# Kernel tuning notes

Hardware: AMD Instinct MI355X
Metric: run time of the kernel (lower is better)

## Reference

```python
import jax, jax.numpy as jnp
import numpy as np
from jax import lax

BATCH = 8192
HIDDEN = 128
N_POINTS = 8
MAX_STEPS = 8     # adaptive substep budget per output interval
RTOL, ATOL = 1e-3, 1e-4

# Dormand-Prince 5(4) tableau (FSAL)
A21 = 1/5
A31, A32 = 3/40, 9/40
A41, A42, A43 = 44/45, -56/15, 32/9
A51, A52, A53, A54 = 19372/6561, -25360/2187, 64448/6561, -212/729
A61, A62, A63, A64, A65 = 9017/3168, -355/33, 46732/5247, 49/176, -5103/18656
B1, B3, B4, B5, B6 = 35/384, 500/1113, 125/192, -2187/6784, 11/84
# error weights = b(5th) - b(4th)
E1 = 35/384 - 5179/57600
E3 = 500/1113 - 7571/16695
E4 = 125/192 - 393/640
E5 = -2187/6784 + 92097/339200
E6 = 11/84 - 187/2100
E7 = -1/40


def setup_inputs() -> dict:
    key = jax.random.key(0)
    ks = jax.random.split(key, 6)
    def xavier(k, fi, fo):
        return (jax.random.normal(k, (fi, fo)) * jnp.sqrt(2.0 / (fi + fo))).astype(jnp.float32)
    W1 = xavier(ks[0], 2, HIDDEN); b1 = jnp.zeros((HIDDEN,), jnp.float32)
    W2 = xavier(ks[1], HIDDEN, HIDDEN); b2 = jnp.zeros((HIDDEN,), jnp.float32)
    W3 = xavier(ks[2], HIDDEN, HIDDEN); b3 = jnp.zeros((HIDDEN,), jnp.float32)
    W4 = xavier(ks[3], HIDDEN, 2); b4 = jnp.zeros((2,), jnp.float32)
    x0 = jax.random.normal(ks[4], (BATCH, 2), jnp.float32)
    t = (jnp.arange(N_POINTS, dtype=jnp.float32) * 0.1)
    return {"x0": x0, "t": t, "W1": W1, "b1": b1, "W2": W2, "b2": b2,
            "W3": W3, "b3": b3, "W4": W4, "b4": b4}


def _odeint(x0, t, W1, b1, W2, b2, W3, b3, W4, b4):
    def f(y):  # autonomous dynamics: ODEFunc ignores t
        h = jax.nn.elu(y @ W1 + b1)
        h = jax.nn.elu(h @ W2 + b2)
        h = jax.nn.elu(h @ W3 + b3)
        return h @ W4 + b4

    def dopri5_step(y, h):
        k1 = f(y)
        k2 = f(y + h * (A21 * k1))
        k3 = f(y + h * (A31 * k1 + A32 * k2))
        k4 = f(y + h * (A41 * k1 + A42 * k2 + A43 * k3))
        k5 = f(y + h * (A51 * k1 + A52 * k2 + A53 * k3 + A54 * k4))
        k6 = f(y + h * (A61 * k1 + A62 * k2 + A63 * k3 + A64 * k4 + A65 * k5))
        y5 = y + h * (B1 * k1 + B3 * k3 + B4 * k4 + B5 * k5 + B6 * k6)
        k7 = f(y5)  # FSAL stage, used only for error estimate here
        err = h * (E1 * k1 + E3 * k3 + E4 * k4 + E5 * k5 + E6 * k6 + E7 * k7)
        tol = ATOL + RTOL * jnp.maximum(jnp.abs(y), jnp.abs(y5))
        err_norm = jnp.sqrt(jnp.mean((err / tol) ** 2))
        return y5, err_norm

    def solve_interval(carry, ts):
        y, h = carry
        t0, t1 = ts

        def body(c, _):
            y, tc, h = c
            remaining = t1 - tc
            done = remaining <= 1e-9
            h_eff = jnp.where(done, h, jnp.minimum(h, remaining))
            y5, err_norm = dopri5_step(y, h_eff)
            accept = (err_norm <= 1.0) & (~done)
            y = jnp.where(accept, y5, y)
            tc = jnp.where(accept, tc + h_eff, tc)
            factor = jnp.clip(0.9 * jnp.maximum(err_norm, 1e-10) ** (-0.2), 0.2, 10.0)
            h = jnp.where(done, h, h_eff * factor)
            return (y, tc, h), None

        (y, _, h), _ = lax.scan(body, (y, t0, h), None, length=MAX_STEPS)
        return (y, h), y

    h0 = (t[1] - t[0]) * 0.5
    (_, _), ys = lax.scan(solve_interval, (x0, h0), (t[:-1], t[1:]))
    return jnp.concatenate([x0[None], ys], axis=0)  # (n_points, batch, 2)


def reference(x0, t, W1, b1, W2, b2, W3, b3, W4, b4):
    return _odeint(x0, t, W1, b1, W2, b2, W3, b3, W4, b4)
```

## Files before the change

### kernel.cpp

```cpp
#include <hip/hip_runtime.h>
#include <stdint.h>

typedef unsigned int u32;
typedef unsigned long long u64;
typedef unsigned short u16;
typedef float f32x4 __attribute__((ext_vector_type(4)));
typedef float f32x2 __attribute__((ext_vector_type(2)));
typedef short short8 __attribute__((ext_vector_type(8)));
typedef unsigned int u32x2 __attribute__((ext_vector_type(2)));
typedef unsigned int u32x4 __attribute__((ext_vector_type(4)));

#define HID  128
#define MT   32
#define NWG  256
#define NTHR 512
#define LD   136

#define OFF_ESUM  0
#define OFF_CNT   512
#define OFF_WPACK 8192
#define OFF_W2TH  16384
#define OFF_W2TL  49152
#define OFF_W3TH  81920
#define OFF_W3TL  114688

constexpr float CA21 = (float)(1.0/5.0);
constexpr float CA31 = (float)(3.0/40.0),   CA32 = (float)(9.0/40.0);
constexpr float CA41 = (float)(44.0/45.0),  CA42 = (float)(-56.0/15.0), CA43 = (float)(32.0/9.0);
constexpr float CA51 = (float)(19372.0/6561.0), CA52 = (float)(-25360.0/2187.0);
constexpr float CA53 = (float)(64448.0/6561.0), CA54 = (float)(-212.0/729.0);
constexpr float CA61 = (float)(9017.0/3168.0),  CA62 = (float)(-355.0/33.0);
constexpr float CA63 = (float)(46732.0/5247.0), CA64 = (float)(49.0/176.0), CA65 = (float)(-5103.0/18656.0);
constexpr float CB1 = (float)(35.0/384.0), CB3 = (float)(500.0/1113.0), CB4 = (float)(125.0/192.0);
constexpr float CB5 = (float)(-2187.0/6784.0), CB6 = (float)(11.0/84.0);
constexpr float CE1 = (float)(35.0/384.0 - 5179.0/57600.0);
constexpr float CE3 = (float)(500.0/1113.0 - 7571.0/16695.0);
constexpr float CE4 = (float)(125.0/192.0 - 393.0/640.0);
constexpr float CE5 = (float)(-2187.0/6784.0 + 92097.0/339200.0);
constexpr float CE6 = (float)(11.0/84.0 - 187.0/2100.0);
constexpr float CE7 = (float)(-1.0/40.0);

template<int N> struct IC { static constexpr int v = N; };

__device__ __forceinline__ u16 f2bf(float x) {
  u32 u = __builtin_bit_cast(u32, x);
  u32 r = (u + 0x7FFFu + ((u >> 16) & 1u)) >> 16;
  return (u16)r;
}
__device__ __forceinline__ float bf2f(u16 b) {
  u32 u = ((u32)b) << 16;
  return __builtin_bit_cast(float, u);
}
__device__ __forceinline__ float eluf(float x) {
  return x > 0.f ? x : (__expf(x) - 1.f);
}
__device__ __forceinline__ u32 cvtpk(float a, float b) {
  u32 r; asm("v_cvt_pk_bf16_f32 %0, %1, %2" : "=v"(r) : "v"(a), "v"(b)); return r;
}

__global__ void prologue(const float* __restrict__ x0, const float* __restrict__ t,
                         const float* __restrict__ W1, const float* __restrict__ b1,
                         const float* __restrict__ W2, const float* __restrict__ b2,
                         const float* __restrict__ W3, const float* __restrict__ b3,
                         const float* __restrict__ W4, const float* __restrict__ b4,
                         float* __restrict__ ws, float* __restrict__ out)
{
  int gid = blockIdx.x * blockDim.x + threadIdx.x;
  out[gid] = x0[gid];
  {
    int k = gid >> 7, j = gid & 127;
    u16* w2th = (u16*)((char*)ws + OFF_W2TH);
    u16* w2tl = (u16*)((char*)ws + OFF_W2TL);
    u16* w3th = (u16*)((char*)ws + OFF_W3TH);
    u16* w3tl = (u16*)((char*)ws + OFF_W3TL);
    float w = W2[gid];
    u16 hb = f2bf(w);
    w2th[j*HID + k] = hb;
    w2tl[j*HID + k] = f2bf(w - bf2f(hb));
    w = W3[gid];
    hb = f2bf(w);
    w3th[j*HID + k] = hb;
    w3tl[j*HID + k] = f2bf(w - bf2f(hb));
  }
  float* wp = ws + OFF_WPACK/4;
  if (gid < 256) wp[gid] = W1[gid];
  if (gid < 128) {
    wp[256 + gid] = b1[gid];
    wp[384 + gid] = b2[gid];
    wp[512 + gid] = b3[gid];
  }
  if (gid < 2)  wp[640 + gid] = b4[gid];
  if (gid < 256) ((u32*)ws)[gid] = 0u;
}

__global__ __launch_bounds__(NTHR, 2)
void solver(const float* __restrict__ x0, const float* __restrict__ t_arr,
            const float* __restrict__ W4g, float* __restrict__ ws,
            float* __restrict__ out)
{
  const int tid  = threadIdx.x;
  const int wg   = blockIdx.x;
  const int lane = tid & 63;
  const int wv   = tid >> 6;
  const int nl   = lane & 15;
  const int g    = lane >> 4;

  __shared__ __align__(16) u16 Ahi[2][MT][LD];
  __shared__ __align__(16) float Wsm[644];
  __shared__ __align__(16) float kS[7][MT][2];
  __shared__ __align__(16) float yL[MT][2];
  __shared__ __align__(16) float y5L[MT][2];
  __shared__ __align__(16) float pD[8][2][16][2];
  __shared__ u32 bcF;
  __shared__ float bcH;

  {
    const float* wp = ws + OFF_WPACK/4;
    Wsm[tid] = wp[tid];
    if (tid < 132) Wsm[512 + tid] = wp[512 + tid];
  }
  if (tid < 64) yL[tid >> 1][tid & 1] = x0[wg*64 + tid];

  const u16* w2th = (const u16*)((const char*)ws + OFF_W2TH);
  const u16* w2tl = (const u16*)((const char*)ws + OFF_W2TL);
  const u16* w3th = (const u16*)((const char*)ws + OFF_W3TH);
  const u16* w3tl = (const u16*)((const char*)ws + OFF_W3TL);
  short8 W2H[4], W2L[4], W3H[4], W3L[4];
  {
    const int nglob = wv*16 + nl;
#pragma unroll
    for (int ks = 0; ks < 4; ++ks) {
      int off = nglob*HID + ks*32 + g*8;
      W2H[ks] = *(const short8*)(w2th + off);
      W2L[ks] = *(const short8*)(w2tl + off);
      W3H[ks] = *(const short8*)(w3th + off);
      W3L[ks] = *(const short8*)(w3tl + off);
    }
  }
  float w4c[4][2];
#pragma unroll
  for (int r = 0; r < 4; ++r) {
    int n = wv*16 + g*4 + r;
    w4c[r][0] = W4g[n*2 + 0];
    w4c[r][1] = W4g[n*2 + 1];
  }
  __syncthreads();
  const f32x4 bv2 = *(const f32x4*)&Wsm[384 + wv*16 + g*4];
  const f32x4 bv3 = *(const f32x4*)&Wsm[512 + wv*16 + g*4];

  u64* esum = (u64*)((char*)ws + OFF_ESUM);
  u32* cnt  = (u32*)((char*)ws + OFF_CNT);

  float h = 0.5f * (t_arr[1] - t_arr[0]);
  float heff = h;

  auto phaseA = [&](auto SC, int fromPD) {
    constexpr int S = decltype(SC)::v;
    const int m  = tid >> 4;
    const int jc = tid & 15;
    float ys0, ys1;
    const float y0 = yL[m][0], y1 = yL[m][1];
    if constexpr (S == 1) {
      ys0 = y0; ys1 = y1;
    } else {
      const int mt = m >> 4, ml = m & 15;
      float kp0, kp1;
      if (S == 2 && !fromPD) {
        kp0 = kS[0][m][0]; kp1 = kS[0][m][1];
      } else {
        kp0 = Wsm[640]; kp1 = Wsm[641];
#pragma unroll
        for (int w = 0; w < 8; ++w) {
          f32x2 p = *(const f32x2*)&pD[w][mt][ml][0];
          kp0 += p[0]; kp1 += p[1];
        }
        if (jc < 2) kS[S-2][m][jc] = jc ? kp1 : kp0;
      }
      if constexpr (S == 2) {
        ys0 = fmaf(heff, CA21*kp0, y0);
        ys1 = fmaf(heff, CA21*kp1, y1);
      } else if constexpr (S == 3) {
        f32x2 k1 = *(const f32x2*)&kS[0][m][0];
        ys0 = fmaf(heff, CA31*k1[0] + CA32*kp0, y0);
        ys1 = fmaf(heff, CA31*k1[1] + CA32*kp1, y1);
      } else if constexpr (S == 4) {
        f32x2 k1 = *(const f32x2*)&kS[0][m][0];
        f32x2 k2 = *(const f32x2*)&kS[1][m][0];
        ys0 = fmaf(heff, CA41*k1[0] + CA42*k2[0] + CA43*kp0, y0);
        ys1 = fmaf(heff, CA41*k1[1] + CA42*k2[1] + CA43*kp1, y1);
      } else if constexpr (S == 5) {
        f32x2 k1 = *(const f32x2*)&kS[0][m][0];
        f32x2 k2 = *(const f32x2*)&kS[1][m][0];
        f32x2 k3 = *(const f32x2*)&kS[2][m][0];
        ys0 = fmaf(heff, CA51*k1[0] + CA52*k2[0] + CA53*k3[0] + CA54*kp0, y0);
        ys1 = fmaf(heff, CA51*k1[1] + CA52*k2[1] + CA53*k3[1] + CA54*kp1, y1);
      } else if constexpr (S == 6) {
        f32x2 k1 = *(const f32x2*)&kS[0][m][0];
        f32x2 k2 = *(const f32x2*)&kS[1][m][0];
        f32x2 k3 = *(const f32x2*)&kS[2][m][0];
        f32x2 k4 = *(const f32x2*)&kS[3][m][0];
        ys0 = fmaf(heff, CA61*k1[0] + CA62*k2[0] + CA63*k3[0] + CA64*k4[0] + CA65*kp0, y0);
        ys1 = fmaf(heff, CA61*k1[1] + CA62*k2[1] + CA63*k3[1] + CA64*k4[1] + CA65*kp1, y1);
      } else {
        f32x2 k1 = *(const f32x2*)&kS[0][m][0];
        f32x2 k3 = *(const f32x2*)&kS[2][m][0];
        f32x2 k4 = *(const f32x2*)&kS[3][m][0];
        f32x2 k5 = *(const f32x2*)&kS[4][m][0];
        ys0 = fmaf(heff, CB1*k1[0] + CB3*k3[0] + CB4*k4[0] + CB5*k5[0] + CB6*kp0, y0);
        ys1 = fmaf(heff, CB1*k1[1] + CB3*k3[1] + CB4*k4[1] + CB5*k5[1] + CB6*kp1, y1);
        if (jc < 2) y5L[m][jc] = jc ? ys1 : ys0;
      }
    }
    const int j0 = jc * 8;
    f32x4 w0a = *(const f32x4*)&Wsm[j0],       w0b = *(const f32x4*)&Wsm[j0 + 4];
    f32x4 w1a = *(const f32x4*)&Wsm[128 + j0], w1b = *(const f32x4*)&Wsm[128 + j0 + 4];
    f32x4 ba  = *(const f32x4*)&Wsm[256 + j0], bb  = *(const f32x4*)&Wsm[256 + j0 + 4];
    float v0 = eluf(fmaf(ys1, w1a[0], fmaf(ys0, w0a[0], ba[0])));
    float v1 = eluf(fmaf(ys1, w1a[1], fmaf(ys0, w0a[1], ba[1])));
    float v2 = eluf(fmaf(ys1, w1a[2], fmaf(ys0, w0a[2], ba[2])));
    float v3 = eluf(fmaf(ys1, w1a[3], fmaf(ys0, w0a[3], ba[3])));
    float v4 = eluf(fmaf(ys1, w1b[0], fmaf(ys0, w0b[0], bb[0])));
    float v5 = eluf(fmaf(ys1, w1b[1], fmaf(ys0, w0b[1], bb[1])));
    float v6 = eluf(fmaf(ys1, w1b[2], fmaf(ys0, w0b[2], bb[2])));
    float v7 = eluf(fmaf(ys1, w1b[3], fmaf(ys0, w0b[3], bb[3])));
    u32x4 hp = {cvtpk(v0,v1), cvtpk(v2,v3), cvtpk(v4,v5), cvtpk(v6,v7)};
    *(u32x4*)&Ahi[0][m][j0] = hp;
  };

  auto mmL2 = [&]() {
    f32x4 a0[2], a1[2];
    a0[0] = bv2; a0[1] = bv2; a1[0] = {0,0,0,0}; a1[1] = {0,0,0,0};
    __builtin_amdgcn_s_setprio(1);
#pragma unroll
    for (int ks = 0; ks < 4; ++ks)
#pragma unroll
      for (int mt = 0; mt < 2; ++mt) {
        short8 bh = *(const short8*)&Ahi[0][mt*16 + nl][ks*32 + g*8];
        a0[mt] = __builtin_amdgcn_mfma_f32_16x16x32_bf16(W2H[ks], bh, a0[mt], 0, 0, 0);
        a1[mt] = __builtin_amdgcn_mfma_f32_16x16x32_bf16(W2L[ks], bh, a1[mt], 0, 0, 0);
      }
    __builtin_amdgcn_s_setprio(0);
    const int n0 = wv*16 + g*4;
#pragma unroll
    for (int mt = 0; mt < 2; ++mt) {
      float v0 = eluf(a0[mt][0] + a1[mt][0]);
      float v1 = eluf(a0[mt][1] + a1[mt][1]);
      float v2 = eluf(a0[mt][2] + a1[mt][2]);
      float v3 = eluf(a0[mt][3] + a1[mt][3]);
      u32x2 hp = {cvtpk(v0, v1), cvtpk(v2, v3)};
      *(u32x2*)&Ahi[1][mt*16 + nl][n0] = hp;
    }
  };

  auto mmL3 = [&]() {
    f32x4 a0[2], a1[2];
    a0[0] = bv3; a0[1] = bv3; a1[0] = {0,0,0,0}; a1[1] = {0,0,0,0};
    __builtin_amdgcn_s_setprio(1);
#pragma unroll
    for (int ks = 0; ks < 4; ++ks)
#pragma unroll
      for (int mt = 0; mt < 2; ++mt) {
        short8 bh = *(const short8*)&Ahi[1][mt*16 + nl][ks*32 + g*8];
        a0[mt] = __builtin_amdgcn_mfma_f32_16x16x32_bf16(W3H[ks], bh, a0[mt], 0, 0, 0);
        a1[mt] = __builtin_amdgcn_mfma_f32_16x16x32_bf16(W3L[ks], bh, a1[mt], 0, 0, 0);
      }
    __builtin_amdgcn_s_setprio(0);
#pragma unroll
    for (int mt = 0; mt < 2; ++mt) {
      float v0 = eluf(a0[mt][0] + a1[mt][0]);
      float v1 = eluf(a0[mt][1] + a1[mt][1]);
      float v2 = eluf(a0[mt][2] + a1[mt][2]);
      float v3 = eluf(a0[mt][3] + a1[mt][3]);
      float p0 = v0*w4c[0][0] + v1*w4c[1][0] + v2*w4c[2][0] + v3*w4c[3][0];
      float p1 = v0*w4c[0][1] + v1*w4c[1][1] + v2*w4c[2][1] + v3*w4c[3][1];
      p0 += __shfl_xor(p0, 16); p0 += __shfl_xor(p0, 32);
      p1 += __shfl_xor(p1, 16); p1 += __shfl_xor(p1, 32);
      if (lane < 16) {
        f32x2 pp = {p0, p1};
        *(f32x2*)&pD[wv][mt][lane][0] = pp;
      }
    }
  };

  for (int iv = 0; iv < 7; ++iv) {
    const float t1 = t_arr[iv + 1];
    float tc = t_arr[iv];
    for (int s = 0; s < 8; ++s) {
      const int step = iv*8 + s;
      float rem = t1 - tc;
      if (rem <= 1e-9f) break;
      heff = fminf(h, rem);

      if (iv == 0 && s == 0) {
        phaseA(IC<1>{}, 0); __syncthreads();
        mmL2(); __syncthreads();
        mmL3(); __syncthreads();
        phaseA(IC<2>{}, 1);
      } else {
        phaseA(IC<2>{}, 0);
      }
      __syncthreads(); mmL2(); __syncthreads(); mmL3(); __syncthreads();
      phaseA(IC<3>{}, 1); __syncthreads(); mmL2(); __syncthreads(); mmL3(); __syncthreads();
      phaseA(IC<4>{}, 1); __syncthreads(); mmL2(); __syncthreads(); mmL3(); __syncthreads();
      phaseA(IC<5>{}, 1); __syncthreads(); mmL2(); __syncthreads(); mmL3(); __syncthreads();
      phaseA(IC<6>{}, 1); __syncthreads(); mmL2(); __syncthreads(); mmL3(); __syncthreads();
      phaseA(IC<7>{}, 1); __syncthreads(); mmL2(); __syncthreads(); mmL3(); __syncthreads();

      if (wv == 0) {
        int m = lane >> 1, c = lane & 1;
        int emt = m >> 4, eml = m & 15;
        float kp = Wsm[640 + c];
#pragma unroll
        for (int w = 0; w < 8; ++w) kp += pD[w][emt][eml][c];
        kS[6][m][c] = kp;
        float e = heff * (CE1*kS[0][m][c] + CE3*kS[2][m][c] + CE4*kS[3][m][c]
                        + CE5*kS[4][m][c] + CE6*kS[5][m][c] + CE7*kp);
        float tol = 1e-4f + 1e-3f * fmaxf(fabsf(yL[m][c]), fabsf(y5L[m][c]));
        float rr = e / tol;
        float es = rr * rr;
#pragma unroll
        for (int mk = 1; mk < 64; mk <<= 1) es += __shfl_xor(es, mk);
        if (lane == 0) {
          if (!(es < 1e8f)) es = 1e8f;
          u64 q = (u64)(es * 1048576.0f);
          __hip_atomic_fetch_add(&esum[step], q, __ATOMIC_RELAXED, __HIP_MEMORY_SCOPE_AGENT);
          __hip_atomic_fetch_add(&cnt[step], 1u, __ATOMIC_RELEASE, __HIP_MEMORY_SCOPE_AGENT);
        }
      }
      if (tid == 0) {
        while (__hip_atomic_load(&cnt[step], __ATOMIC_ACQUIRE, __HIP_MEMORY_SCOPE_AGENT) < (u32)NWG)
          __builtin_amdgcn_s_sleep(1);
        u64 q = __hip_atomic_load(&esum[step], __ATOMIC_RELAXED, __HIP_MEMORY_SCOPE_AGENT);
        float sum = (float)q * (1.0f/1048576.0f);
        float err_norm = sqrtf(sum * (1.0f/16384.f));
        bool acc = (err_norm <= 1.0f);
        float factor = fminf(10.f, fmaxf(0.2f, 0.9f * powf(fmaxf(err_norm, 1e-10f), -0.2f)));
        bcF = acc ? 1u : 0u;
        bcH = heff * factor;
      }
      __syncthreads();
      {
        bool acc = bcF != 0u;
        if (acc) {
          if (tid < 64) { int m = tid >> 1, c = tid & 1;
            yL[m][c] = y5L[m][c];
            kS[0][m][c] = kS[6][m][c];
          }
          tc += heff;
        }
        h = bcH;
      }
      __syncthreads();
    }
    if (tid < 64)
      out[(size_t)(iv + 1) * 16384 + wg*64 + tid] = yL[tid >> 1][tid & 1];
  }
}

extern "C" void kernel_launch(void* const* d_in, const int* in_sizes, int n_in,
                              void* d_out, int out_size, void* d_ws, size_t ws_size,
                              hipStream_t stream)
{
  const float* x0 = (const float*)d_in[0];
  const float* t  = (const float*)d_in[1];
  const float* W1 = (const float*)d_in[2];
  const float* b1 = (const float*)d_in[3];
  const float* W2 = (const float*)d_in[4];
  const float* b2 = (const float*)d_in[5];
  const float* W3 = (const float*)d_in[6];
  const float* b3 = (const float*)d_in[7];
  const float* W4 = (const float*)d_in[8];
  const float* b4 = (const float*)d_in[9];
  float* out = (float*)d_out;
  float* ws  = (float*)d_ws;

  prologue<<<64, 256, 0, stream>>>(x0, t, W1, b1, W2, b2, W3, b3, W4, b4, ws, out);
  solver<<<NWG, NTHR, 0, stream>>>(x0, t, W4, ws, out);
}
```

Measured before the change: 205.8 us.

## Drop bf16 hi/lo weight split and remove per-step trailing barrier

Replaces the two-term bf16 hi/lo weight decomposition for the hidden layers with a single bf16 copy, halving the MFMA work and the weight registers held per thread, and drops the wave priority hints. It also remaps which threads commit the accepted state so that each thread updates the rows it later reads itself, which lets the barrier at the end of every substep move out to the end of each interval. The precision loss on the weights may change error norms and therefore the accept/reject decisions and step sizes, and the barrier removal depends on that thread-to-row mapping matching the stage code.

```diff
diff --git a/kernel.cpp b/kernel.cpp
--- a/kernel.cpp
+++ b/kernel.cpp
@@ -20,9 +20,7 @@
 #define OFF_CNT   512
 #define OFF_WPACK 8192
 #define OFF_W2TH  16384
-#define OFF_W2TL  49152
-#define OFF_W3TH  81920
-#define OFF_W3TL  114688
+#define OFF_W3TH  49152
 
 constexpr float CA21 = (float)(1.0/5.0);
 constexpr float CA31 = (float)(3.0/40.0),   CA32 = (float)(9.0/40.0);
@@ -47,10 +45,6 @@
   u32 r = (u + 0x7FFFu + ((u >> 16) & 1u)) >> 16;
   return (u16)r;
 }
-__device__ __forceinline__ float bf2f(u16 b) {
-  u32 u = ((u32)b) << 16;
-  return __builtin_bit_cast(float, u);
-}
 __device__ __forceinline__ float eluf(float x) {
   return x > 0.f ? x : (__expf(x) - 1.f);
 }
@@ -70,17 +64,9 @@
   {
     int k = gid >> 7, j = gid & 127;
     u16* w2th = (u16*)((char*)ws + OFF_W2TH);
-    u16* w2tl = (u16*)((char*)ws + OFF_W2TL);
     u16* w3th = (u16*)((char*)ws + OFF_W3TH);
-    u16* w3tl = (u16*)((char*)ws + OFF_W3TL);
-    float w = W2[gid];
-    u16 hb = f2bf(w);
-    w2th[j*HID + k] = hb;
-    w2tl[j*HID + k] = f2bf(w - bf2f(hb));
-    w = W3[gid];
-    hb = f2bf(w);
-    w3th[j*HID + k] = hb;
-    w3tl[j*HID + k] = f2bf(w - bf2f(hb));
+    w2th[j*HID + k] = f2bf(W2[gid]);
+    w3th[j*HID + k] = f2bf(W3[gid]);
   }
   float* wp = ws + OFF_WPACK/4;
   if (gid < 256) wp[gid] = W1[gid];
@@ -122,19 +108,15 @@
   if (tid < 64) yL[tid >> 1][tid & 1] = x0[wg*64 + tid];
 
   const u16* w2th = (const u16*)((const char*)ws + OFF_W2TH);
-  const u16* w2tl = (const u16*)((const char*)ws + OFF_W2TL);
   const u16* w3th = (const u16*)((const char*)ws + OFF_W3TH);
-  const u16* w3tl = (const u16*)((const char*)ws + OFF_W3TL);
-  short8 W2H[4], W2L[4], W3H[4], W3L[4];
+  short8 W2H[4], W3H[4];
   {
     const int nglob = wv*16 + nl;
 #pragma unroll
     for (int ks = 0; ks < 4; ++ks) {
       int off = nglob*HID + ks*32 + g*8;
       W2H[ks] = *(const short8*)(w2th + off);
-      W2L[ks] = *(const short8*)(w2tl + off);
       W3H[ks] = *(const short8*)(w3th + off);
-      W3L[ks] = *(const short8*)(w3tl + off);
     }
   }
   float w4c[4][2];
@@ -228,49 +210,43 @@
   };
 
   auto mmL2 = [&]() {
-    f32x4 a0[2], a1[2];
-    a0[0] = bv2; a0[1] = bv2; a1[0] = {0,0,0,0}; a1[1] = {0,0,0,0};
-    __builtin_amdgcn_s_setprio(1);
+    f32x4 a0[2];
+    a0[0] = bv2; a0[1] = bv2;
 #pragma unroll
     for (int ks = 0; ks < 4; ++ks)
 #pragma unroll
       for (int mt = 0; mt < 2; ++mt) {
         short8 bh = *(const short8*)&Ahi[0][mt*16 + nl][ks*32 + g*8];
         a0[mt] = __builtin_amdgcn_mfma_f32_16x16x32_bf16(W2H[ks], bh, a0[mt], 0, 0, 0);
-        a1[mt] = __builtin_amdgcn_mfma_f32_16x16x32_bf16(W2L[ks], bh, a1[mt], 0, 0, 0);
-      }
-    __builtin_amdgcn_s_setprio(0);
+      }
     const int n0 = wv*16 + g*4;
 #pragma unroll
     for (int mt = 0; mt < 2; ++mt) {
-      float v0 = eluf(a0[mt][0] + a1[mt][0]);
-      float v1 = eluf(a0[mt][1] + a1[mt][1]);
-      float v2 = eluf(a0[mt][2] + a1[mt][2]);
-      float v3 = eluf(a0[mt][3] + a1[mt][3]);
+      float v0 = eluf(a0[mt][0]);
+      float v1 = eluf(a0[mt][1]);
+      float v2 = eluf(a0[mt][2]);
+      float v3 = eluf(a0[mt][3]);
       u32x2 hp = {cvtpk(v0, v1), cvtpk(v2, v3)};
       *(u32x2*)&Ahi[1][mt*16 + nl][n0] = hp;
     }
   };
 
   auto mmL3 = [&]() {
-    f32x4 a0[2], a1[2];
-    a0[0] = bv3; a0[1] = bv3; a1[0] = {0,0,0,0}; a1[1] = {0,0,0,0};
-    __builtin_amdgcn_s_setprio(1);
+    f32x4 a0[2];
+    a0[0] = bv3; a0[1] = bv3;
 #pragma unroll
     for (int ks = 0; ks < 4; ++ks)
 #pragma unroll
       for (int mt = 0; mt < 2; ++mt) {
         short8 bh = *(const short8*)&Ahi[1][mt*16 + nl][ks*32 + g*8];
         a0[mt] = __builtin_amdgcn_mfma_f32_16x16x32_bf16(W3H[ks], bh, a0[mt], 0, 0, 0);
-        a1[mt] = __builtin_amdgcn_mfma_f32_16x16x32_bf16(W3L[ks], bh, a1[mt], 0, 0, 0);
-      }
-    __builtin_amdgcn_s_setprio(0);
+      }
 #pragma unroll
     for (int mt = 0; mt < 2; ++mt) {
-      float v0 = eluf(a0[mt][0] + a1[mt][0]);
-      float v1 = eluf(a0[mt][1] + a1[mt][1]);
-      float v2 = eluf(a0[mt][2] + a1[mt][2]);
-      float v3 = eluf(a0[mt][3] + a1[mt][3]);
+      float v0 = eluf(a0[mt][0]);
+      float v1 = eluf(a0[mt][1]);
+      float v2 = eluf(a0[mt][2]);
+      float v3 = eluf(a0[mt][3]);
       float p0 = v0*w4c[0][0] + v1*w4c[1][0] + v2*w4c[2][0] + v3*w4c[3][0];
       float p1 = v0*w4c[0][1] + v1*w4c[1][1] + v2*w4c[2][1] + v3*w4c[3][1];
       p0 += __shfl_xor(p0, 16); p0 += __shfl_xor(p0, 32);
@@ -342,16 +318,17 @@
       {
         bool acc = bcF != 0u;
         if (acc) {
-          if (tid < 64) { int m = tid >> 1, c = tid & 1;
-            yL[m][c] = y5L[m][c];
-            kS[0][m][c] = kS[6][m][c];
+          int m = tid >> 4, jc = tid & 15;
+          if (jc < 2) {
+            yL[m][jc] = y5L[m][jc];
+            kS[0][m][jc] = kS[6][m][jc];
           }
           tc += heff;
         }
         h = bcH;
       }
-      __syncthreads();
-    }
+    }
+    __syncthreads();
     if (tid < 64)
       out[(size_t)(iv + 1) * 16384 + wg*64 + tid] = yL[tid >> 1][tid & 1];
   }
```

New measurement: 198.9 us. -3.4%, faster.
